# Kernel tuning notes

Hardware: AMD Instinct MI355X
Metric: run time of the kernel (lower is better)

## Reference

```python
import jax, jax.numpy as jnp
import numpy as np

N_SEQ, N_WIN, OUT_DIM = 4096, 128, 128
N_REAL_LEN = 100000

def setup_inputs() -> dict:
    key = jax.random.key(0)
    k1, k2 = jax.random.split(key)
    TRFs = jax.random.normal(k1, (N_SEQ, N_WIN, OUT_DIM), dtype=jnp.float32)
    sourceIdx = jnp.sort(jax.random.randint(k2, (N_SEQ,), 0, N_REAL_LEN))
    return {"TRFs": TRFs, "sourceIdx": sourceIdx, "nRealLen": N_REAL_LEN}

def reference(TRFs, sourceIdx, nRealLen):
    # TRFs: (nSeq, nWin, outDim); sourceIdx: (nSeq,) in [0, nRealLen)
    # Original builds a (outDim, nWin, nRealLen) cache via index scatter, then
    # fold (col2im) overlap-adds: out[d, s+k] += TRFs[seq, k, d] for sourceIdx[seq]=s.
    # Equivalent direct scatter-add of each TRF window at its onset index.
    nSeq, nWin, outDim = TRFs.shape
    idx = sourceIdx[:, None] + jnp.arange(nWin)[None, :]  # (nSeq, nWin) target times
    acc = jnp.zeros((nRealLen + nWin - 1, outDim), dtype=TRFs.dtype)
    acc = acc.at[idx].add(TRFs)                           # scatter-add windows
    return acc[:nRealLen].T                               # (outDim, nRealLen)
```

## Files before the change

kernel.cpp:

```cpp
#include <hip/hip_runtime.h>


#define T_TILE  32
#define OUT_DIM 128
#define N_WIN   128

__global__ __launch_bounds__(OUT_DIM, 4) void trf_gather_kernel(
    const float* __restrict__ TRFs,
    const int*   __restrict__ sourceIdx,
    int nSeq, int nRealLen,
    float* __restrict__ out)
{
    const int d  = threadIdx.x;
    const int t0 = blockIdx.x * T_TILE;
    if (t0 >= nRealLen) return;

    int lo;
    {
        int target = t0 - (N_WIN - 1);
        int a = 0, b = nSeq;
        while (a < b) { int m = (a + b) >> 1; if (sourceIdx[m] < target) a = m + 1; else b = m; }
        lo = a;
    }
    int hi;
    {
        int target = t0 + T_TILE;
        int a = lo, b = nSeq;
        while (a < b) { int m = (a + b) >> 1; if (sourceIdx[m] < target) a = m + 1; else b = m; }
        hi = a;
    }

    float acc[T_TILE];
#pragma unroll
    for (int i = 0; i < T_TILE; ++i) acc[i] = 0.f;

    for (int seq = lo; seq < hi; ++seq) {
        int s = sourceIdx[seq];
        const float* row = TRFs + (size_t)seq * (N_WIN * OUT_DIM) + d;
        const int base = t0 - s;

        float v[T_TILE];
#pragma unroll
        for (int i = 0; i < T_TILE; ++i) {
            int k  = base + i;
            int kc = k < 0 ? 0 : (k > (N_WIN - 1) ? (N_WIN - 1) : k);
            v[i] = row[kc * OUT_DIM];
        }
#pragma unroll
        for (int i = 0; i < T_TILE; ++i) {
            int k = base + i;
            acc[i] += (k >= 0 && k < N_WIN) ? v[i] : 0.0f;
        }
    }

    float* o = out + (size_t)d * nRealLen + t0;
    const int tmax = nRealLen - t0;
    if (tmax >= T_TILE && (nRealLen & 3) == 0 && (t0 & 3) == 0) {
#pragma unroll
        for (int i = 0; i < T_TILE; i += 4) {
            float4 v4 = make_float4(acc[i], acc[i + 1], acc[i + 2], acc[i + 3]);
            *reinterpret_cast<float4*>(o + i) = v4;
        }
    } else {
        for (int i = 0; i < T_TILE && i < tmax; ++i) o[i] = acc[i];
    }
}

extern "C" void kernel_launch(void* const* d_in, const int* in_sizes, int n_in,
                              void* d_out, int out_size, void* d_ws, size_t ws_size,
                              hipStream_t stream) {
    const float* TRFs      = (const float*)d_in[0];
    const int*   sourceIdx = (const int*)d_in[1];
    const int    nSeq      = in_sizes[1];
    const int    nRealLen  = out_size / OUT_DIM;

    const int nBlocks = (nRealLen + T_TILE - 1) / T_TILE;
    trf_gather_kernel<<<nBlocks, OUT_DIM, 0, stream>>>(
        TRFs, sourceIdx, nSeq, nRealLen, (float*)d_out);
}
```

Baseline: 388.2 us.

## Remap threads to float4 dim groups with time sub-tiles and double-buffered prefetch

Threads are remapped so each one handles four consecutive output dims, loaded as a float4, over an 8-step time sub-tile. Previously each thread handled one dim over the full 32-step tile. TRF reads become 16-byte vector loads, and the loads for the next sequence are software-prefetched into a second register buffer while the current one accumulates. The cost is more register pressure from the two float4 buffers. The output stores are now spread across four rows per thread, which may lower store coalescing.

```diff
diff --git a/kernel.cpp b/kernel.cpp
--- a/kernel.cpp
+++ b/kernel.cpp
@@ -2,17 +2,21 @@
 
 
 #define T_TILE  32
+#define T_SUB   8
 #define OUT_DIM 128
 #define N_WIN   128
 
-__global__ __launch_bounds__(OUT_DIM, 4) void trf_gather_kernel(
+__global__ __launch_bounds__(128, 4) void trf_gather_kernel(
     const float* __restrict__ TRFs,
     const int*   __restrict__ sourceIdx,
     int nSeq, int nRealLen,
     float* __restrict__ out)
 {
-    const int d  = threadIdx.x;
-    const int t0 = blockIdx.x * T_TILE;
+    const int tid = threadIdx.x;
+    const int dg  = tid & 31;
+    const int st  = tid >> 5;
+    const int t0  = blockIdx.x * T_TILE;
+    const int tb  = t0 + st * T_SUB;
     if (t0 >= nRealLen) return;
 
     int lo;
@@ -30,39 +34,69 @@
         hi = a;
     }
 
-    float acc[T_TILE];
+    float4 acc[T_SUB];
 #pragma unroll
-    for (int i = 0; i < T_TILE; ++i) acc[i] = 0.f;
+    for (int i = 0; i < T_SUB; ++i) acc[i] = make_float4(0.f, 0.f, 0.f, 0.f);
 
-    for (int seq = lo; seq < hi; ++seq) {
+    const char* tbase = (const char*)TRFs + (size_t)dg * 16;
+
+    auto prefetch = [&](float4* buf, int seq, int& s_out) {
         int s = sourceIdx[seq];
-        const float* row = TRFs + (size_t)seq * (N_WIN * OUT_DIM) + d;
-        const int base = t0 - s;
+        s_out = s;
+        const char* row = tbase + (size_t)seq * (N_WIN * OUT_DIM * 4);
+#pragma unroll
+        for (int i = 0; i < T_SUB; ++i) {
+            int k  = tb + i - s;
+            int kc = k < 0 ? 0 : (k > (N_WIN - 1) ? (N_WIN - 1) : k);
+            buf[i] = *(const float4*)(row + (size_t)kc * (OUT_DIM * 4));
+        }
+    };
+    auto accum = [&](const float4* buf, int s) {
+#pragma unroll
+        for (int i = 0; i < T_SUB; ++i) {
+            int k = tb + i - s;
+            float m = ((unsigned)k < (unsigned)N_WIN) ? 1.0f : 0.0f;
+            acc[i].x += m * buf[i].x;
+            acc[i].y += m * buf[i].y;
+            acc[i].z += m * buf[i].z;
+            acc[i].w += m * buf[i].w;
+        }
+    };
 
-        float v[T_TILE];
-#pragma unroll
-        for (int i = 0; i < T_TILE; ++i) {
-            int k  = base + i;
-            int kc = k < 0 ? 0 : (k > (N_WIN - 1) ? (N_WIN - 1) : k);
-            v[i] = row[kc * OUT_DIM];
+    if (lo < hi) {
+        float4 bufA[T_SUB], bufB[T_SUB];
+        int sA, sB;
+        int q = lo;
+        prefetch(bufA, q, sA);
+        while (q + 1 < hi) {
+            prefetch(bufB, q + 1, sB);
+            accum(bufA, sA);
+            ++q;
+            if (q + 1 < hi) {
+                prefetch(bufA, q + 1, sA);
+                accum(bufB, sB);
+                ++q;
+            } else {
+                accum(bufB, sB);
+                ++q;
+            }
         }
-#pragma unroll
-        for (int i = 0; i < T_TILE; ++i) {
-            int k = base + i;
-            acc[i] += (k >= 0 && k < N_WIN) ? v[i] : 0.0f;
-        }
+        if (q < hi) accum(bufA, sA);
     }
 
-    float* o = out + (size_t)d * nRealLen + t0;
-    const int tmax = nRealLen - t0;
-    if (tmax >= T_TILE && (nRealLen & 3) == 0 && (t0 & 3) == 0) {
 #pragma unroll
-        for (int i = 0; i < T_TILE; i += 4) {
-            float4 v4 = make_float4(acc[i], acc[i + 1], acc[i + 2], acc[i + 3]);
-            *reinterpret_cast<float4*>(o + i) = v4;
+    for (int j = 0; j < 4; ++j) {
+        float r[T_SUB];
+#pragma unroll
+        for (int i = 0; i < T_SUB; ++i) r[i] = ((const float*)&acc[i])[j];
+        float* orow = out + (size_t)(4 * dg + j) * nRealLen + tb;
+        if (tb + T_SUB <= nRealLen) {
+            *(float4*)(orow + 0) = make_float4(r[0], r[1], r[2], r[3]);
+            *(float4*)(orow + 4) = make_float4(r[4], r[5], r[6], r[7]);
+        } else {
+            for (int i = 0; i < T_SUB; ++i)
+                if (tb + i < nRealLen) orow[i] = r[i];
         }
-    } else {
-        for (int i = 0; i < T_TILE && i < tmax; ++i) o[i] = acc[i];
     }
 }
 
@@ -75,6 +109,6 @@
     const int    nRealLen  = out_size / OUT_DIM;
 
     const int nBlocks = (nRealLen + T_TILE - 1) / T_TILE;
-    trf_gather_kernel<<<nBlocks, OUT_DIM, 0, stream>>>(
+    trf_gather_kernel<<<nBlocks, 128, 0, stream>>>(
         TRFs, sourceIdx, nSeq, nRealLen, (float*)d_out);
 }
```

Measured after the change: 433.3 us. +11.6%, slower.
